# Optimization experiments

Hardware: AMD Instinct MI355X
Metric: run time of the kernel (lower is better)

Reference implementation:

```python
import jax, jax.numpy as jnp
import numpy as np

N_NODES = 50000
N_EDGES = 800000
IN_CH = 128
HID = 64
HEADS = 4
OUT_CH = 64
NEG_SLOPE = 0.2


def _add_self_loops(ei, n):
    loops = jnp.tile(jnp.arange(n, dtype=ei.dtype)[None, :], (2, 1))
    return jnp.concatenate([ei, loops], axis=1)


def _gat_conv(x, ei, W, a_s, a_d, b, concat):
    """PyG-style GATConv. x:[N,F], ei:[2,E], W:[F,H*C], a_s/a_d:[H,C]."""
    N = x.shape[0]
    H, C = a_s.shape
    h = (x @ W).reshape(N, H, C)                     # [N,H,C]
    src, dst = ei[0], ei[1]
    al_s = (h * a_s[None]).sum(-1)                   # [N,H]
    al_d = (h * a_d[None]).sum(-1)                   # [N,H]
    logits = jax.nn.leaky_relu(al_s[src] + al_d[dst], NEG_SLOPE)  # [E,H]
    # segment softmax over incoming edges of each dst node
    m = jax.ops.segment_max(logits, dst, num_segments=N)
    m = jax.lax.stop_gradient(jnp.where(jnp.isfinite(m), m, 0.0))
    ex = jnp.exp(logits - m[dst])
    denom = jax.ops.segment_sum(ex, dst, num_segments=N)
    alpha = ex / (denom[dst] + 1e-16)                # [E,H]
    out = jax.ops.segment_sum(alpha[:, :, None] * h[src], dst, num_segments=N)  # [N,H,C]
    out = out.reshape(N, H * C) if concat else out.mean(axis=1)
    return out + b


def _hetero_layer(x, edges, self_loop_flags, W, a_s, a_d, b, concat):
    N = x.shape[0]
    out = None
    for r in range(3):
        ei = _add_self_loops(edges[r], N) if self_loop_flags[r] else edges[r]
        o = _gat_conv(x, ei, W[r], a_s[r], a_d[r], b[r], concat)
        out = o if out is None else out + o
    return out


def setup_inputs() -> dict:
    key = jax.random.key(0)
    ks = jax.random.split(key, 16)
    s = 0.05
    return {
        "x": jax.random.normal(ks[0], (N_NODES, IN_CH), jnp.float32),
        "e_blocks": jax.random.randint(ks[1], (2, N_EDGES), 0, N_NODES),
        "e_spatial": jax.random.randint(ks[2], (2, N_EDGES), 0, N_NODES),
        "e_similar": jax.random.randint(ks[3], (2, N_EDGES), 0, N_NODES),
        "W1": jax.random.normal(ks[4], (3, IN_CH, HEADS * HID), jnp.float32) * s,
        "a1s": jax.random.normal(ks[5], (3, HEADS, HID), jnp.float32) * s,
        "a1d": jax.random.normal(ks[6], (3, HEADS, HID), jnp.float32) * s,
        "b1": jax.random.normal(ks[7], (3, HEADS * HID), jnp.float32) * s,
        "W2": jax.random.normal(ks[8], (3, HEADS * HID, HEADS * HID), jnp.float32) * s,
        "a2s": jax.random.normal(ks[9], (3, HEADS, HID), jnp.float32) * s,
        "a2d": jax.random.normal(ks[10], (3, HEADS, HID), jnp.float32) * s,
        "b2": jax.random.normal(ks[11], (3, HID), jnp.float32) * s,
        "Wl": jax.random.normal(ks[12], (HID, OUT_CH), jnp.float32) * s,
        "bl": jax.random.normal(ks[13], (OUT_CH,), jnp.float32) * s,
    }


def reference(x, e_blocks, e_spatial, e_similar, W1, a1s, a1d, b1,
              W2, a2s, a2d, b2, Wl, bl):
    edges = [e_blocks, e_spatial, e_similar]
    self_loops = [False, True, True]  # 'blocks' has add_self_loops=False
    h = _hetero_layer(x, edges, self_loops, W1, a1s, a1d, b1, concat=True)
    h = jax.nn.relu(h)
    h = _hetero_layer(h, edges, self_loops, W2, a2s, a2d, b2, concat=False)
    h = jax.nn.relu(h)
    return h @ Wl + bl
```

## Files before the change

kernel.cpp:

```cpp
#include <hip/hip_runtime.h>
#include <hip/hip_bf16.h>
#include <hip/hip_fp16.h>

#define NN 50000
#define NE 800000
#define FIN 128
#define HCC 256
#define OC 64
#define NSL 0.2f
#define NT3 (3 * NN)

typedef __attribute__((ext_vector_type(8))) short sh8;
typedef __attribute__((ext_vector_type(16))) float f32x16;

struct __attribute__((aligned(8))) h4 { __half x, y, z, w; };
struct __attribute__((aligned(8))) s4 { short x, y, z, w; };

__device__ __forceinline__ unsigned short bf_rne(float f) {
  unsigned u = __float_as_uint(f);
  u += 0x7FFF + ((u >> 16) & 1);
  return (unsigned short)(u >> 16);
}

__device__ __forceinline__ float edge_w(float lg) {
  lg = (lg > 0.f) ? lg : NSL * lg;
  return __expf(lg);
}

template<int KK>
__global__ __launch_bounds__(256) void k_prep(const float* __restrict__ W,
                                              short* __restrict__ out) {
  int i = blockIdx.x * 256 + threadIdx.x;
  if (i >= 3 * KK * 256) return;
  int r = i / (KK * 256);
  int rem = i - r * KK * 256;
  int k = rem >> 8;
  int n = rem & 255;
  float f = W[i];
  unsigned short hb = bf_rne(f);
  float hf = __uint_as_float(((unsigned)hb) << 16);
  unsigned short lb = bf_rne(f - hf);
  int cb = n >> 7, c = n & 127, ks8 = k >> 3, kj = k & 7;
  size_t base = (size_t)r * 4 * KK * 128;
  size_t oh = base + ((size_t)((cb * 2 + 0) * (KK / 8) + ks8) * 128 + c) * 8 + kj;
  size_t ol = base + ((size_t)((cb * 2 + 1) * (KK / 8) + ks8) * 128 + c) * 8 + kj;
  out[oh] = (short)hb;
  out[ol] = (short)lb;
}

__global__ __launch_bounds__(256) void k_split(const float* __restrict__ x,
                                               short* __restrict__ xhi,
                                               short* __restrict__ xlo) {
  int i = blockIdx.x * 256 + threadIdx.x;
  if (i >= NN * FIN / 4) return;
  float4 v = ((const float4*)x)[i];
  s4 h, l;
  float f, hf;
  f = v.x; h.x = (short)bf_rne(f); hf = __uint_as_float(((unsigned)(unsigned short)h.x) << 16); l.x = (short)bf_rne(f - hf);
  f = v.y; h.y = (short)bf_rne(f); hf = __uint_as_float(((unsigned)(unsigned short)h.y) << 16); l.y = (short)bf_rne(f - hf);
  f = v.z; h.z = (short)bf_rne(f); hf = __uint_as_float(((unsigned)(unsigned short)h.z) << 16); l.z = (short)bf_rne(f - hf);
  f = v.w; h.w = (short)bf_rne(f); hf = __uint_as_float(((unsigned)(unsigned short)h.w) << 16); l.w = (short)bf_rne(f - hf);
  ((s4*)xhi)[i] = h;
  ((s4*)xlo)[i] = l;
}

__global__ void k_hist3(const int* __restrict__ e0, const int* __restrict__ e1,
                        const int* __restrict__ e2, int* __restrict__ deg3) {
  int i = blockIdx.x * blockDim.x + threadIdx.x;
  int st = gridDim.x * blockDim.x;
  for (; i < 3 * NE; i += st) {
    int rel = i / NE;
    int j = i - rel * NE;
    const int* e = (rel == 0) ? e0 : ((rel == 1) ? e1 : e2);
    atomicAdd(&deg3[rel * NN + e[NE + j]], 1);
  }
}

__global__ __launch_bounds__(1024) void k_bsum(const int* __restrict__ deg3,
                                               int* __restrict__ bsum) {
  __shared__ int s[1024];
  int t = threadIdx.x;
  int i = blockIdx.x * 1024 + t;
  s[t] = (i < NT3) ? deg3[i] : 0;
  __syncthreads();
  for (int off = 512; off > 0; off >>= 1) {
    if (t < off) s[t] += s[t + off];
    __syncthreads();
  }
  if (t == 0) bsum[blockIdx.x] = s[0];
}

__global__ __launch_bounds__(256) void k_scan2(const int* __restrict__ bsum,
                                               int* __restrict__ boffs, int nb) {
  __shared__ int s[256];
  int t = threadIdx.x;
  int v = (t < nb) ? bsum[t] : 0;
  s[t] = v;
  __syncthreads();
  for (int off = 1; off < 256; off <<= 1) {
    int x = (t >= off) ? s[t - off] : 0;
    __syncthreads();
    s[t] += x;
    __syncthreads();
  }
  if (t < nb) boffs[t] = s[t] - v;
}

__global__ __launch_bounds__(1024) void k_rowptr(const int* __restrict__ deg3,
                                                 const int* __restrict__ boffs,
                                                 int* __restrict__ rpA,
                                                 int* __restrict__ cursor3) {
  __shared__ int s[1024];
  int t = threadIdx.x;
  int i = blockIdx.x * 1024 + t;
  int d = (i < NT3) ? deg3[i] : 0;
  s[t] = d;
  __syncthreads();
  for (int off = 1; off < 1024; off <<= 1) {
    int x = (t >= off) ? s[t - off] : 0;
    __syncthreads();
    s[t] += x;
    __syncthreads();
  }
  if (i < NT3) {
    int excl = boffs[blockIdx.x] + s[t] - d;
    int r = (i < NN) ? 0 : ((i < 2 * NN) ? 1 : 2);
    int n = i - r * NN;
    int val = excl - r * NE;
    rpA[r * (NN + 1) + n] = val;
    cursor3[i] = val;
  }
  if (blockIdx.x == 0 && t < 3) rpA[t * (NN + 1) + NN] = NE;
}

__global__ void k_scatter3(const int* __restrict__ e0, const int* __restrict__ e1,
                           const int* __restrict__ e2, int* __restrict__ cursor3,
                           int* __restrict__ csAll) {
  int i = blockIdx.x * blockDim.x + threadIdx.x;
  int st = gridDim.x * blockDim.x;
  for (; i < 3 * NE; i += st) {
    int rel = i / NE;
    int j = i - rel * NE;
    const int* e = (rel == 0) ? e0 : ((rel == 1) ? e1 : e2);
    int pos = atomicAdd(&cursor3[rel * NN + e[NE + j]], 1);
    csAll[(size_t)rel * NE + pos] = e[j];
  }
}

template<int KK>
__global__ __launch_bounds__(256) void k_mgemm(const short* __restrict__ Ahi,
                                               const short* __restrict__ Alo,
                                               const short* __restrict__ BcAll,
                                               const float* __restrict__ asfAll,
                                               const float* __restrict__ adfAll,
                                               __half* __restrict__ houtAll,
                                               float* __restrict__ alsAll,
                                               float* __restrict__ aldAll, int M) {
  const int rel = blockIdx.y;
  const short* Bc = BcAll + (size_t)rel * 4 * KK * 128;
  const float* asf = asfAll + rel * HCC;
  const float* adf = adfAll + rel * HCC;
  __half* hout = houtAll + (size_t)rel * NN * HCC;
  float* als = alsAll + (size_t)rel * NN * 4;
  float* ald = aldAll + (size_t)rel * NN * 4;

  const int tid = threadIdx.x;
  const int lane = tid & 63;
  const int w = tid >> 6;
  const int l31 = lane & 31;
  const int lg = lane >> 5;
  const int wrow = blockIdx.x * 64 + (w & 1) * 32;
  const int ch = w >> 1;

  f32x16 acc[4];
#pragma unroll
  for (int t = 0; t < 4; ++t) acc[t] = (f32x16)(0.f);

  const int r = wrow + l31;
  const bool aok = r < M;
  const short* ahp = Ahi + (size_t)r * KK;
  const short* alp = Alo + (size_t)r * KK;
  const short* bh = Bc + (size_t)(ch * 2 + 0) * KK * 128 + l31 * 8;
  const short* bl = Bc + (size_t)(ch * 2 + 1) * KK * 128 + l31 * 8;

#pragma unroll 2
  for (int kst = 0; kst < KK / 16; ++kst) {
    const int k0 = kst * 16 + lg * 8;
    sh8 ahi = {0, 0, 0, 0, 0, 0, 0, 0}, alo = ahi;
    if (aok) {
      ahi = *(const sh8*)(ahp + k0);
      alo = *(const sh8*)(alp + k0);
    }
    const int ks8 = kst * 2 + lg;
    const short* bhp = bh + (size_t)ks8 * 1024;
    const short* blp = bl + (size_t)ks8 * 1024;
    sh8 bhf[4], blf[4];
#pragma unroll
    for (int t = 0; t < 4; ++t) {
      bhf[t] = *(const sh8*)(bhp + t * 256);
      blf[t] = *(const sh8*)(blp + t * 256);
    }
#pragma unroll
    for (int t = 0; t < 4; ++t) {
      acc[t] = __builtin_amdgcn_mfma_f32_32x32x16_bf16(ahi, bhf[t], acc[t], 0, 0, 0);
      acc[t] = __builtin_amdgcn_mfma_f32_32x32x16_bf16(alo, bhf[t], acc[t], 0, 0, 0);
      acc[t] = __builtin_amdgcn_mfma_f32_32x32x16_bf16(ahi, blf[t], acc[t], 0, 0, 0);
    }
  }

  float asr[4], adr[4];
#pragma unroll
  for (int t = 0; t < 4; ++t) {
    int col = ch * 128 + t * 32 + l31;
    asr[t] = asf[col];
    adr[t] = adf[col];
  }
#pragma unroll
  for (int v = 0; v < 16; ++v) {
    const int rl = (v & 3) + 8 * (v >> 2) + 4 * lg;
    const int row = wrow + rl;
    const bool rok = row < M;
    float s0 = 0.f, s1 = 0.f, d0 = 0.f, d1 = 0.f;
    __half* hp = hout + (size_t)row * 256 + ch * 128 + l31;
#pragma unroll
    for (int t = 0; t < 4; ++t) {
      float dv = acc[t][v];
      if (rok) hp[t * 32] = __float2half(dv);
      if (t < 2) { s0 += dv * asr[t]; d0 += dv * adr[t]; }
      else       { s1 += dv * asr[t]; d1 += dv * adr[t]; }
    }
#pragma unroll
    for (int m = 1; m < 32; m <<= 1) {
      s0 += __shfl_xor(s0, m);
      s1 += __shfl_xor(s1, m);
      d0 += __shfl_xor(d0, m);
      d1 += __shfl_xor(d1, m);
    }
    if (rok && l31 == 0) {
      *(float2*)(als + (size_t)row * 4 + ch * 2) = make_float2(s0, s1);
      *(float2*)(ald + (size_t)row * 4 + ch * 2) = make_float2(d0, d1);
    }
  }
}

__global__ __launch_bounds__(256) void k_ew3(const float* __restrict__ als3,
                                             const float* __restrict__ ald3,
                                             const int* __restrict__ rpA,
                                             const int* __restrict__ csAll,
                                             float* __restrict__ ew3,
                                             float* __restrict__ wsum3,
                                             float* __restrict__ ewself3) {
  int wid = (blockIdx.x * 256 + threadIdx.x) >> 6;
  int lane = threadIdx.x & 63;
  if (wid >= NT3) return;
  int rel = wid / NN;
  int n = wid - rel * NN;
  const int* cs = csAll + (size_t)rel * NE;
  const float* als = als3 + (size_t)rel * NN * 4;
  const float* ald = ald3 + (size_t)rel * NN * 4;
  float* ew = ew3 + (size_t)rel * NE * 4;
  int rs = rpA[rel * (NN + 1) + n];
  int re = rpA[rel * (NN + 1) + n + 1];
  int head = lane & 3;
  int el = lane >> 2;
  float ad = ald[n * 4 + head];
  float ws = 0.f;
  for (int base = rs; base < re; base += 16) {
    int e = base + el;
    float w = 0.f;
    if (e < re) {
      int s = cs[e];
      w = edge_w(als[s * 4 + head] + ad);
      ew[(size_t)e * 4 + head] = w;
    }
    ws += w;
  }
  ws += __shfl_xor(ws, 4);
  ws += __shfl_xor(ws, 8);
  ws += __shfl_xor(ws, 16);
  ws += __shfl_xor(ws, 32);
  float wself = 0.f;
  if (rel > 0) wself = edge_w(als[n * 4 + head] + ad);
  if (lane < 4) {
    ewself3[((size_t)rel * NN + n) * 4 + head] = wself;
    wsum3[((size_t)rel * NN + n) * 4 + head] = ws + wself;
  }
}

template<bool SL>
__device__ __forceinline__ void gat_rel(int n, int head, size_t loff,
                                        const __half* __restrict__ h,
                                        const float* __restrict__ ew,
                                        const float* __restrict__ wsum,
                                        const float* __restrict__ ewself,
                                        const int* __restrict__ rp,
                                        const int* __restrict__ cs,
                                        float& ox, float& oy, float& oz, float& ow) {
  int rs = rp[n], re = rp[n + 1];
  float ax = 0.f, ay = 0.f, az = 0.f, aw = 0.f;
  int i = rs;
  for (; i + 8 <= re; i += 8) {
    int s[8];
#pragma unroll
    for (int j = 0; j < 8; ++j) s[j] = cs[i + j];
    float w[8];
#pragma unroll
    for (int j = 0; j < 8; ++j) w[j] = ew[(size_t)(i + j) * 4 + head];
    h4 v[8];
#pragma unroll
    for (int j = 0; j < 8; ++j) v[j] = *(const h4*)&h[(size_t)s[j] * HCC + loff];
#pragma unroll
    for (int j = 0; j < 8; ++j) {
      ax = fmaf(w[j], __half2float(v[j].x), ax);
      ay = fmaf(w[j], __half2float(v[j].y), ay);
      az = fmaf(w[j], __half2float(v[j].z), az);
      aw = fmaf(w[j], __half2float(v[j].w), aw);
    }
  }
  for (; i < re; ++i) {
    int s = cs[i];
    float w = ew[(size_t)i * 4 + head];
    h4 hv = *(const h4*)&h[(size_t)s * HCC + loff];
    ax = fmaf(w, __half2float(hv.x), ax);
    ay = fmaf(w, __half2float(hv.y), ay);
    az = fmaf(w, __half2float(hv.z), az);
    aw = fmaf(w, __half2float(hv.w), aw);
  }
  if (SL) {
    float w = ewself[n * 4 + head];
    h4 hv = *(const h4*)&h[(size_t)n * HCC + loff];
    ax = fmaf(w, __half2float(hv.x), ax);
    ay = fmaf(w, __half2float(hv.y), ay);
    az = fmaf(w, __half2float(hv.z), az);
    aw = fmaf(w, __half2float(hv.w), aw);
  }
  float inv = 1.0f / (wsum[n * 4 + head] + 1e-16f);
  ox = fmaf(ax, inv, ox);
  oy = fmaf(ay, inv, oy);
  oz = fmaf(az, inv, oz);
  ow = fmaf(aw, inv, ow);
}

template<bool CONCAT>
__global__ __launch_bounds__(256) void k_gather3(const __half* __restrict__ h3,
                                                 const float* __restrict__ ew3,
                                                 const float* __restrict__ wsum3,
                                                 const float* __restrict__ ewself3,
                                                 const int* __restrict__ rpA,
                                                 const int* __restrict__ csAll,
                                                 const float* __restrict__ bias,
                                                 short* __restrict__ o1hi,
                                                 short* __restrict__ o1lo,
                                                 float* __restrict__ o32) {
  int gid = blockIdx.x * blockDim.x + threadIdx.x;
  int n = gid >> 6;
  int lane = threadIdx.x & 63;
  if (n >= NN) return;
  int head = lane >> 4;
  size_t loff = (size_t)lane * 4;
  const size_t HS = (size_t)NN * HCC;
  const size_t AS = (size_t)NN * 4;
  const size_t ES = (size_t)NE * 4;
  float ox = 0.f, oy = 0.f, oz = 0.f, ow = 0.f;
  gat_rel<false>(n, head, loff, h3,          ew3,          wsum3,          ewself3,          rpA,                csAll,          ox, oy, oz, ow);
  gat_rel<true >(n, head, loff, h3 + HS,     ew3 + ES,     wsum3 + AS,     ewself3 + AS,     rpA + (NN + 1),     csAll + NE,     ox, oy, oz, ow);
  gat_rel<true >(n, head, loff, h3 + 2 * HS, ew3 + 2 * ES, wsum3 + 2 * AS, ewself3 + 2 * AS, rpA + 2 * (NN + 1), csAll + 2 * NE, ox, oy, oz, ow);
  if (CONCAT) {
    float4 b0 = *(const float4*)&bias[lane * 4];
    float4 b1 = *(const float4*)&bias[HCC + lane * 4];
    float4 b2 = *(const float4*)&bias[2 * HCC + lane * 4];
    float vv[4];
    vv[0] = fmaxf(ox + b0.x + b1.x + b2.x, 0.f);
    vv[1] = fmaxf(oy + b0.y + b1.y + b2.y, 0.f);
    vv[2] = fmaxf(oz + b0.z + b1.z + b2.z, 0.f);
    vv[3] = fmaxf(ow + b0.w + b1.w + b2.w, 0.f);
    s4 hv, lv;
    short* hp = (short*)&hv;
    short* lp = (short*)&lv;
#pragma unroll
    for (int j = 0; j < 4; ++j) {
      unsigned short hb = bf_rne(vv[j]);
      float hf = __uint_as_float(((unsigned)hb) << 16);
      hp[j] = (short)hb;
      lp[j] = (short)bf_rne(vv[j] - hf);
    }
    *(s4*)&o1hi[(size_t)n * HCC + loff] = hv;
    *(s4*)&o1lo[(size_t)n * HCC + loff] = lv;
  } else {
    ox += __shfl_xor(ox, 16); oy += __shfl_xor(oy, 16);
    oz += __shfl_xor(oz, 16); ow += __shfl_xor(ow, 16);
    ox += __shfl_xor(ox, 32); oy += __shfl_xor(oy, 32);
    oz += __shfl_xor(oz, 32); ow += __shfl_xor(ow, 32);
    if (lane < 16) {
      float4 b0 = *(const float4*)&bias[lane * 4];
      float4 b1 = *(const float4*)&bias[OC + lane * 4];
      float4 b2 = *(const float4*)&bias[2 * OC + lane * 4];
      float4 o;
      o.x = 0.25f * ox + b0.x + b1.x + b2.x;
      o.y = 0.25f * oy + b0.y + b1.y + b2.y;
      o.z = 0.25f * oz + b0.z + b1.z + b2.z;
      o.w = 0.25f * ow + b0.w + b1.w + b2.w;
      *(float4*)&o32[(size_t)n * OC + lane * 4] = o;
    }
  }
}

__global__ __launch_bounds__(256) void k_final(const float* __restrict__ out2,
                                               const float* __restrict__ Wl,
                                               const float* __restrict__ bl,
                                               float* __restrict__ outp) {
  __shared__ float Ws[64 * 64];
  __shared__ float bs[64];
  int tid = threadIdx.x;
  for (int i = tid; i < 4096; i += 256) Ws[i] = Wl[i];
  if (tid < 64) bs[tid] = bl[tid];
  __syncthreads();
  int r = blockIdx.x * 4 + (tid >> 6);
  int c = tid & 63;
  if (r >= NN) return;
  const float* xr = &out2[(size_t)r * OC];
  float acc = bs[c];
#pragma unroll
  for (int k = 0; k < 64; ++k) {
    float xv = xr[k];
    xv = (xv > 0.f) ? xv : 0.f;
    acc = fmaf(xv, Ws[k * 64 + c], acc);
  }
  outp[(size_t)r * OC + c] = acc;
}

extern "C" void kernel_launch(void* const* d_in, const int* in_sizes, int n_in,
                              void* d_out, int out_size, void* d_ws, size_t ws_size,
                              hipStream_t stream) {
  const float* x   = (const float*)d_in[0];
  const int* e_b   = (const int*)d_in[1];
  const int* e_sp  = (const int*)d_in[2];
  const int* e_si  = (const int*)d_in[3];
  const float* W1  = (const float*)d_in[4];
  const float* a1s = (const float*)d_in[5];
  const float* a1d = (const float*)d_in[6];
  const float* b1  = (const float*)d_in[7];
  const float* W2  = (const float*)d_in[8];
  const float* a2s = (const float*)d_in[9];
  const float* a2d = (const float*)d_in[10];
  const float* b2  = (const float*)d_in[11];
  const float* Wl  = (const float*)d_in[12];
  const float* bl  = (const float*)d_in[13];
  float* out = (float*)d_out;

  char* ws = (char*)d_ws;
  size_t off = 0;
  auto alloc = [&](size_t b) {
    char* p = ws + off;
    off += (b + 255) & ~(size_t)255;
    return p;
  };
  __half* h3  = (__half*)alloc((size_t)3 * NN * HCC * 2);
  short* o1hi = (short*)alloc((size_t)NN * HCC * 2);
  short* o1lo = (short*)alloc((size_t)NN * HCC * 2);
  float* out2 = (float*)o1hi;
  char* U = alloc((size_t)3 * NE * 4 * 4);
  short* xhi = (short*)U;
  short* xlo = (short*)(U + (size_t)NN * FIN * 2);
  float* ew3 = (float*)U;
  float* als3 = (float*)alloc((size_t)3 * NN * 4 * 4);
  float* ald3 = (float*)alloc((size_t)3 * NN * 4 * 4);
  float* wsum3 = (float*)alloc((size_t)3 * NN * 4 * 4);
  float* ewself3 = (float*)alloc((size_t)3 * NN * 4 * 4);
  int* deg3    = (int*)alloc((size_t)NT3 * 4);
  int* cursor3 = (int*)alloc((size_t)NT3 * 4);
  int* rpA     = (int*)alloc((size_t)3 * (NN + 1) * 4);
  int* bsum    = (int*)alloc(256 * 4);
  int* boffs   = (int*)alloc(256 * 4);
  short* Wc1   = (short*)alloc((size_t)3 * 4 * FIN * 128 * 2);
  short* Wc2   = (short*)alloc((size_t)3 * 4 * HCC * 128 * 2);
  int* csAll   = (int*)alloc((size_t)3 * NE * 4);

  k_prep<FIN><<<(3 * FIN * 256 + 255) / 256, 256, 0, stream>>>(W1, Wc1);
  k_prep<HCC><<<(3 * HCC * 256 + 255) / 256, 256, 0, stream>>>(W2, Wc2);
  k_split<<<(NN * FIN / 4 + 255) / 256, 256, 0, stream>>>(x, xhi, xlo);

  hipMemsetAsync(deg3, 0, (size_t)NT3 * 4, stream);
  k_hist3<<<2048, 256, 0, stream>>>(e_b, e_sp, e_si, deg3);
  const int NB = (NT3 + 1023) / 1024;
  k_bsum<<<NB, 1024, 0, stream>>>(deg3, bsum);
  k_scan2<<<1, 256, 0, stream>>>(bsum, boffs, NB);
  k_rowptr<<<NB, 1024, 0, stream>>>(deg3, boffs, rpA, cursor3);
  k_scatter3<<<2048, 256, 0, stream>>>(e_b, e_sp, e_si, cursor3, csAll);

  const int gblocks = (NN + 63) / 64;
  const int ablocks = (NN * 64) / 256;
  const int eblocks = (NT3 + 3) / 4;

  k_mgemm<FIN><<<dim3(gblocks, 3), 256, 0, stream>>>(
      xhi, xlo, Wc1, a1s, a1d, h3, als3, ald3, NN);
  k_ew3<<<eblocks, 256, 0, stream>>>(als3, ald3, rpA, csAll, ew3, wsum3, ewself3);
  k_gather3<true><<<ablocks, 256, 0, stream>>>(
      h3, ew3, wsum3, ewself3, rpA, csAll, b1, o1hi, o1lo, nullptr);

  k_mgemm<HCC><<<dim3(gblocks, 3), 256, 0, stream>>>(
      o1hi, o1lo, Wc2, a2s, a2d, h3, als3, ald3, NN);
  k_ew3<<<eblocks, 256, 0, stream>>>(als3, ald3, rpA, csAll, ew3, wsum3, ewself3);
  k_gather3<false><<<ablocks, 256, 0, stream>>>(
      h3, ew3, wsum3, ewself3, rpA, csAll, b2, nullptr, nullptr, out2);

  k_final<<<(NN + 3) / 4, 256, 0, stream>>>(out2, Wl, bl, out);
}
```

Before: 1.008 ms.

## Fuse edge-weight computation into gather kernel and split scatter per relation

Removes the separate k_ew3 pass, which computed per-edge attention weights and per-node sums into global buffers. The gather kernel now recomputes each edge weight from als/ald inline and accumulates the softmax denominator itself, eliminating the write and re-read of a 3*NE*4 float buffer. The cost is extra exp work in the gather, which is redundant across the 16 lanes per head, plus an extra random read of als per edge. Separately, the combined scatter kernel is replaced by three per-relation launches without the divide and select.

New measurement: 940.2 us. -6.8%, faster.

```diff
diff --git a/kernel.cpp b/kernel.cpp
--- a/kernel.cpp
+++ b/kernel.cpp
@@ -133,17 +133,13 @@
   if (blockIdx.x == 0 && t < 3) rpA[t * (NN + 1) + NN] = NE;
 }
 
-__global__ void k_scatter3(const int* __restrict__ e0, const int* __restrict__ e1,
-                           const int* __restrict__ e2, int* __restrict__ cursor3,
-                           int* __restrict__ csAll) {
+__global__ void k_scatter(const int* __restrict__ srcv, const int* __restrict__ dstv,
+                          int* __restrict__ cursor, int* __restrict__ csr_src, int n) {
   int i = blockIdx.x * blockDim.x + threadIdx.x;
   int st = gridDim.x * blockDim.x;
-  for (; i < 3 * NE; i += st) {
-    int rel = i / NE;
-    int j = i - rel * NE;
-    const int* e = (rel == 0) ? e0 : ((rel == 1) ? e1 : e2);
-    int pos = atomicAdd(&cursor3[rel * NN + e[NE + j]], 1);
-    csAll[(size_t)rel * NE + pos] = e[j];
+  for (; i < n; i += st) {
+    int pos = atomicAdd(&cursor[dstv[i]], 1);
+    csr_src[pos] = srcv[i];
   }
 }
 
@@ -243,83 +239,42 @@
   }
 }
 
-__global__ __launch_bounds__(256) void k_ew3(const float* __restrict__ als3,
-                                             const float* __restrict__ ald3,
-                                             const int* __restrict__ rpA,
-                                             const int* __restrict__ csAll,
-                                             float* __restrict__ ew3,
-                                             float* __restrict__ wsum3,
-                                             float* __restrict__ ewself3) {
-  int wid = (blockIdx.x * 256 + threadIdx.x) >> 6;
-  int lane = threadIdx.x & 63;
-  if (wid >= NT3) return;
-  int rel = wid / NN;
-  int n = wid - rel * NN;
-  const int* cs = csAll + (size_t)rel * NE;
-  const float* als = als3 + (size_t)rel * NN * 4;
-  const float* ald = ald3 + (size_t)rel * NN * 4;
-  float* ew = ew3 + (size_t)rel * NE * 4;
-  int rs = rpA[rel * (NN + 1) + n];
-  int re = rpA[rel * (NN + 1) + n + 1];
-  int head = lane & 3;
-  int el = lane >> 2;
-  float ad = ald[n * 4 + head];
-  float ws = 0.f;
-  for (int base = rs; base < re; base += 16) {
-    int e = base + el;
-    float w = 0.f;
-    if (e < re) {
-      int s = cs[e];
-      w = edge_w(als[s * 4 + head] + ad);
-      ew[(size_t)e * 4 + head] = w;
-    }
-    ws += w;
-  }
-  ws += __shfl_xor(ws, 4);
-  ws += __shfl_xor(ws, 8);
-  ws += __shfl_xor(ws, 16);
-  ws += __shfl_xor(ws, 32);
-  float wself = 0.f;
-  if (rel > 0) wself = edge_w(als[n * 4 + head] + ad);
-  if (lane < 4) {
-    ewself3[((size_t)rel * NN + n) * 4 + head] = wself;
-    wsum3[((size_t)rel * NN + n) * 4 + head] = ws + wself;
-  }
-}
-
 template<bool SL>
 __device__ __forceinline__ void gat_rel(int n, int head, size_t loff,
                                         const __half* __restrict__ h,
-                                        const float* __restrict__ ew,
-                                        const float* __restrict__ wsum,
-                                        const float* __restrict__ ewself,
+                                        const float* __restrict__ als,
+                                        const float* __restrict__ ald,
                                         const int* __restrict__ rp,
                                         const int* __restrict__ cs,
                                         float& ox, float& oy, float& oz, float& ow) {
+  float ad = ald[n * 4 + head];
   int rs = rp[n], re = rp[n + 1];
-  float ax = 0.f, ay = 0.f, az = 0.f, aw = 0.f;
+  float ax = 0.f, ay = 0.f, az = 0.f, aw = 0.f, wsum = 0.f;
   int i = rs;
   for (; i + 8 <= re; i += 8) {
     int s[8];
 #pragma unroll
     for (int j = 0; j < 8; ++j) s[j] = cs[i + j];
-    float w[8];
-#pragma unroll
-    for (int j = 0; j < 8; ++j) w[j] = ew[(size_t)(i + j) * 4 + head];
+    float al[8];
+#pragma unroll
+    for (int j = 0; j < 8; ++j) al[j] = als[s[j] * 4 + head];
     h4 v[8];
 #pragma unroll
     for (int j = 0; j < 8; ++j) v[j] = *(const h4*)&h[(size_t)s[j] * HCC + loff];
 #pragma unroll
     for (int j = 0; j < 8; ++j) {
-      ax = fmaf(w[j], __half2float(v[j].x), ax);
-      ay = fmaf(w[j], __half2float(v[j].y), ay);
-      az = fmaf(w[j], __half2float(v[j].z), az);
-      aw = fmaf(w[j], __half2float(v[j].w), aw);
+      float w = edge_w(al[j] + ad);
+      wsum += w;
+      ax = fmaf(w, __half2float(v[j].x), ax);
+      ay = fmaf(w, __half2float(v[j].y), ay);
+      az = fmaf(w, __half2float(v[j].z), az);
+      aw = fmaf(w, __half2float(v[j].w), aw);
     }
   }
   for (; i < re; ++i) {
     int s = cs[i];
-    float w = ew[(size_t)i * 4 + head];
+    float w = edge_w(als[s * 4 + head] + ad);
+    wsum += w;
     h4 hv = *(const h4*)&h[(size_t)s * HCC + loff];
     ax = fmaf(w, __half2float(hv.x), ax);
     ay = fmaf(w, __half2float(hv.y), ay);
@@ -327,14 +282,15 @@
     aw = fmaf(w, __half2float(hv.w), aw);
   }
   if (SL) {
-    float w = ewself[n * 4 + head];
+    float w = edge_w(als[n * 4 + head] + ad);
+    wsum += w;
     h4 hv = *(const h4*)&h[(size_t)n * HCC + loff];
     ax = fmaf(w, __half2float(hv.x), ax);
     ay = fmaf(w, __half2float(hv.y), ay);
     az = fmaf(w, __half2float(hv.z), az);
     aw = fmaf(w, __half2float(hv.w), aw);
   }
-  float inv = 1.0f / (wsum[n * 4 + head] + 1e-16f);
+  float inv = 1.0f / (wsum + 1e-16f);
   ox = fmaf(ax, inv, ox);
   oy = fmaf(ay, inv, oy);
   oz = fmaf(az, inv, oz);
@@ -343,9 +299,8 @@
 
 template<bool CONCAT>
 __global__ __launch_bounds__(256) void k_gather3(const __half* __restrict__ h3,
-                                                 const float* __restrict__ ew3,
-                                                 const float* __restrict__ wsum3,
-                                                 const float* __restrict__ ewself3,
+                                                 const float* __restrict__ als3,
+                                                 const float* __restrict__ ald3,
                                                  const int* __restrict__ rpA,
                                                  const int* __restrict__ csAll,
                                                  const float* __restrict__ bias,
@@ -360,11 +315,10 @@
   size_t loff = (size_t)lane * 4;
   const size_t HS = (size_t)NN * HCC;
   const size_t AS = (size_t)NN * 4;
-  const size_t ES = (size_t)NE * 4;
   float ox = 0.f, oy = 0.f, oz = 0.f, ow = 0.f;
-  gat_rel<false>(n, head, loff, h3,          ew3,          wsum3,          ewself3,          rpA,                csAll,          ox, oy, oz, ow);
-  gat_rel<true >(n, head, loff, h3 + HS,     ew3 + ES,     wsum3 + AS,     ewself3 + AS,     rpA + (NN + 1),     csAll + NE,     ox, oy, oz, ow);
-  gat_rel<true >(n, head, loff, h3 + 2 * HS, ew3 + 2 * ES, wsum3 + 2 * AS, ewself3 + 2 * AS, rpA + 2 * (NN + 1), csAll + 2 * NE, ox, oy, oz, ow);
+  gat_rel<false>(n, head, loff, h3,          als3,          ald3,          rpA,                csAll,          ox, oy, oz, ow);
+  gat_rel<true >(n, head, loff, h3 + HS,     als3 + AS,     ald3 + AS,     rpA + (NN + 1),     csAll + NE,     ox, oy, oz, ow);
+  gat_rel<true >(n, head, loff, h3 + 2 * HS, als3 + 2 * AS, ald3 + 2 * AS, rpA + 2 * (NN + 1), csAll + 2 * NE, ox, oy, oz, ow);
   if (CONCAT) {
     float4 b0 = *(const float4*)&bias[lane * 4];
     float4 b1 = *(const float4*)&bias[HCC + lane * 4];
@@ -459,14 +413,10 @@
   short* o1hi = (short*)alloc((size_t)NN * HCC * 2);
   short* o1lo = (short*)alloc((size_t)NN * HCC * 2);
   float* out2 = (float*)o1hi;
-  char* U = alloc((size_t)3 * NE * 4 * 4);
-  short* xhi = (short*)U;
-  short* xlo = (short*)(U + (size_t)NN * FIN * 2);
-  float* ew3 = (float*)U;
+  short* xhi  = (short*)alloc((size_t)NN * FIN * 2);
+  short* xlo  = (short*)alloc((size_t)NN * FIN * 2);
   float* als3 = (float*)alloc((size_t)3 * NN * 4 * 4);
   float* ald3 = (float*)alloc((size_t)3 * NN * 4 * 4);
-  float* wsum3 = (float*)alloc((size_t)3 * NN * 4 * 4);
-  float* ewself3 = (float*)alloc((size_t)3 * NN * 4 * 4);
   int* deg3    = (int*)alloc((size_t)NT3 * 4);
   int* cursor3 = (int*)alloc((size_t)NT3 * 4);
   int* rpA     = (int*)alloc((size_t)3 * (NN + 1) * 4);
@@ -476,6 +426,8 @@
   short* Wc2   = (short*)alloc((size_t)3 * 4 * HCC * 128 * 2);
   int* csAll   = (int*)alloc((size_t)3 * NE * 4);
 
+  const int* edges[3] = {e_b, e_sp, e_si};
+
   k_prep<FIN><<<(3 * FIN * 256 + 255) / 256, 256, 0, stream>>>(W1, Wc1);
   k_prep<HCC><<<(3 * HCC * 256 + 255) / 256, 256, 0, stream>>>(W2, Wc2);
   k_split<<<(NN * FIN / 4 + 255) / 256, 256, 0, stream>>>(x, xhi, xlo);
@@ -486,23 +438,22 @@
   k_bsum<<<NB, 1024, 0, stream>>>(deg3, bsum);
   k_scan2<<<1, 256, 0, stream>>>(bsum, boffs, NB);
   k_rowptr<<<NB, 1024, 0, stream>>>(deg3, boffs, rpA, cursor3);
-  k_scatter3<<<2048, 256, 0, stream>>>(e_b, e_sp, e_si, cursor3, csAll);
+  for (int r = 0; r < 3; ++r)
+    k_scatter<<<1024, 256, 0, stream>>>(edges[r], edges[r] + NE, cursor3 + r * NN,
+                                        csAll + (size_t)r * NE, NE);
 
   const int gblocks = (NN + 63) / 64;
   const int ablocks = (NN * 64) / 256;
-  const int eblocks = (NT3 + 3) / 4;
 
   k_mgemm<FIN><<<dim3(gblocks, 3), 256, 0, stream>>>(
       xhi, xlo, Wc1, a1s, a1d, h3, als3, ald3, NN);
-  k_ew3<<<eblocks, 256, 0, stream>>>(als3, ald3, rpA, csAll, ew3, wsum3, ewself3);
   k_gather3<true><<<ablocks, 256, 0, stream>>>(
-      h3, ew3, wsum3, ewself3, rpA, csAll, b1, o1hi, o1lo, nullptr);
+      h3, als3, ald3, rpA, csAll, b1, o1hi, o1lo, nullptr);
 
   k_mgemm<HCC><<<dim3(gblocks, 3), 256, 0, stream>>>(
       o1hi, o1lo, Wc2, a2s, a2d, h3, als3, ald3, NN);
-  k_ew3<<<eblocks, 256, 0, stream>>>(als3, ald3, rpA, csAll, ew3, wsum3, ewself3);
   k_gather3<false><<<ablocks, 256, 0, stream>>>(
-      h3, ew3, wsum3, ewself3, rpA, csAll, b2, nullptr, nullptr, out2);
+      h3, als3, ald3, rpA, csAll, b2, nullptr, nullptr, out2);
 
   k_final<<<(NN + 3) / 4, 256, 0, stream>>>(out2, Wl, bl, out);
 }
```
